# Kernel tuning notes

Hardware: AMD Instinct MI355X
Metric: run time of the kernel (lower is better)

Reference implementation:

```python
import jax, jax.numpy as jnp
import numpy as np

IM_SIZE = (384, 384)
GRID_OVERSAMP = 1.25
GRID_SIZE = tuple(round(s * GRID_OVERSAMP) for s in IM_SIZE)  # (480, 480)
N, C, K = 1, 16, 500000


def setup_inputs() -> dict:
    key = jax.random.key(0)
    k1, k2, k3 = jax.random.split(key, 3)
    img_real = jax.random.normal(k1, (N, C) + IM_SIZE, dtype=jnp.float32)
    img_imag = jax.random.normal(k2, (N, C) + IM_SIZE, dtype=jnp.float32)
    # continuous k-space trajectory coords in [-s/2, s/2) per dim
    u = jax.random.uniform(k3, (N, K, 2), dtype=jnp.float32)
    trj = (u - 0.5) * jnp.asarray(IM_SIZE, dtype=jnp.float32)
    return {"img_real": img_real, "img_imag": img_imag, "trj": trj}


def _rescale_trajectory(trj):
    # trj * oversamp, shift to [0, gs-1], round -> int32 grid indices
    gs = jnp.asarray(GRID_SIZE, dtype=jnp.float32)
    trj_rs = trj * GRID_OVERSAMP
    trj_rs = jnp.clip(trj_rs + gs / 2, 0.0, gs - 1)
    return jnp.round(trj_rs).astype(jnp.int32)


def _forward_complex(img, idx):
    # PadLast: center-pad last d dims from im_size to grid size
    pads = [((g - s) // 2, g - s - (g - s) // 2) for g, s in zip(GRID_SIZE, IM_SIZE)]
    img_os = jnp.pad(img, ((0, 0), (0, 0), pads[0], pads[1]))
    # sp_fft: centered orthonormal FFT over spatial dims
    axes = (-2, -1)
    ksp_os = jnp.fft.fftshift(
        jnp.fft.fftn(jnp.fft.ifftshift(img_os, axes=axes), axes=axes, norm="ortho"),
        axes=axes,
    )  # (N, C, Gx, Gy) complex64
    # per-batch irregular gather at rounded grid indices (multi_index)
    gather = jax.vmap(lambda k, t: k[:, t[:, 0], t[:, 1]])(ksp_os, idx)  # (N, C, K)
    return gather


def reference(img_real, img_imag, trj):
    img = (img_real + 1j * img_imag).astype(jnp.complex64)
    idx = _rescale_trajectory(trj)
    ksp = _forward_complex(img, idx)
    # return real/imag stacked so output is a float tensor: (2, N, C, K)
    return jnp.stack([ksp.real, ksp.imag]).astype(jnp.float32)
```

## Files before the change

### kernel.cpp

```cpp
#include <hip/hip_runtime.h>
#include <math.h>

#define PI_F 3.14159265358979323846f
#define LROW 489

__device__ __forceinline__ void wave_sync() {
  __builtin_amdgcn_wave_barrier();
  asm volatile("" ::: "memory");
}

__device__ __forceinline__ void dft2(float* vr, float* vi) {
  float ar = vr[0], ai = vi[0];
  vr[0] = ar + vr[1]; vi[0] = ai + vi[1];
  vr[1] = ar - vr[1]; vi[1] = ai - vi[1];
}

__device__ __forceinline__ void dft3(float* vr, float* vi) {
  const float s3 = 0.86602540378443864676f;
  float t1r = vr[1] + vr[2], t1i = vi[1] + vi[2];
  float t2r = vr[1] - vr[2], t2i = vi[1] - vi[2];
  float ar = vr[0] - 0.5f * t1r, ai = vi[0] - 0.5f * t1i;
  float br = s3 * t2r, bi = s3 * t2i;
  vr[0] = vr[0] + t1r; vi[0] = vi[0] + t1i;
  vr[1] = ar + bi; vi[1] = ai - br;
  vr[2] = ar - bi; vi[2] = ai + br;
}

__device__ __forceinline__ void dft4(float* vr, float* vi) {
  float t0r = vr[0] + vr[2], t0i = vi[0] + vi[2];
  float t1r = vr[0] - vr[2], t1i = vi[0] - vi[2];
  float t2r = vr[1] + vr[3], t2i = vi[1] + vi[3];
  float t3r = vr[1] - vr[3], t3i = vi[1] - vi[3];
  vr[0] = t0r + t2r; vi[0] = t0i + t2i;
  vr[2] = t0r - t2r; vi[2] = t0i - t2i;
  vr[1] = t1r + t3i; vi[1] = t1i - t3r;
  vr[3] = t1r - t3i; vi[3] = t1i + t3r;
}

__device__ __forceinline__ void dft5(float* vr, float* vi) {
  const float c1 = 0.30901699437494742410f, s1 = 0.95105651629515357212f;
  const float c2 = -0.80901699437494742410f, s2 = 0.58778525229247312917f;
  float t1r = vr[1] + vr[4], t1i = vi[1] + vi[4];
  float t2r = vr[2] + vr[3], t2i = vi[2] + vi[3];
  float t3r = vr[1] - vr[4], t3i = vi[1] - vi[4];
  float t4r = vr[2] - vr[3], t4i = vi[2] - vi[3];
  float a1r = vr[0] + c1 * t1r + c2 * t2r, a1i = vi[0] + c1 * t1i + c2 * t2i;
  float a2r = vr[0] + c2 * t1r + c1 * t2r, a2i = vi[0] + c2 * t1i + c1 * t2i;
  float b1r = s1 * t3r + s2 * t4r, b1i = s1 * t3i + s2 * t4i;
  float b2r = s2 * t3r - s1 * t4r, b2i = s2 * t3i - s1 * t4i;
  vr[0] = vr[0] + t1r + t2r; vi[0] = vi[0] + t1i + t2i;
  vr[1] = a1r + b1i; vi[1] = a1i - b1r;
  vr[4] = a1r - b1i; vi[4] = a1i + b1r;
  vr[2] = a2r + b2i; vi[2] = a2i - b2r;
  vr[3] = a2r - b2i; vi[3] = a2i + b2r;
}

__device__ __forceinline__ void dft8(float* vr, float* vi) {
  float er[4]  = {vr[0], vr[2], vr[4], vr[6]};
  float ei[4]  = {vi[0], vi[2], vi[4], vi[6]};
  float or_[4] = {vr[1], vr[3], vr[5], vr[7]};
  float oi[4]  = {vi[1], vi[3], vi[5], vi[7]};
  dft4(er, ei); dft4(or_, oi);
  const float h = 0.70710678118654752440f;
  float t1r = h * (or_[1] + oi[1]), t1i = h * (oi[1] - or_[1]);
  float t2r = oi[2],                t2i = -or_[2];
  float t3r = h * (oi[3] - or_[3]), t3i = -h * (or_[3] + oi[3]);
  vr[0] = er[0] + or_[0]; vi[0] = ei[0] + oi[0];
  vr[4] = er[0] - or_[0]; vi[4] = ei[0] - oi[0];
  vr[1] = er[1] + t1r;    vi[1] = ei[1] + t1i;
  vr[5] = er[1] - t1r;    vi[5] = ei[1] - t1i;
  vr[2] = er[2] + t2r;    vi[2] = ei[2] + t2i;
  vr[6] = er[2] - t2r;    vi[6] = ei[2] - t2i;
  vr[3] = er[3] + t3r;    vi[3] = ei[3] + t3i;
  vr[7] = er[3] - t3r;    vi[7] = ei[3] - t3i;
}

template <int R, int Ls>
__device__ __forceinline__ void fft_stage_ip(float2* s, int lane) {
  constexpr int M = 480 / R;
  constexpr int NI = (M + 63) / 64;
  const float w = -2.0f * PI_F / (float)(Ls * R);
  float vr[NI][R], vi[NI][R];
#pragma unroll
  for (int t = 0; t < NI; ++t) {
    const int i = lane + t * 64;
    if (i < M) {
#pragma unroll
      for (int r = 0; r < R; ++r) {
        float2 x = s[i + r * M];
        vr[t][r] = x.x; vi[t][r] = x.y;
      }
    }
  }
  asm volatile("" ::: "memory");
#pragma unroll
  for (int t = 0; t < NI; ++t) {
    const int i = lane + t * 64;
    if (i < M) {
      const int j = i % Ls, k = i / Ls;
      if constexpr (Ls > 1) {
#pragma unroll
        for (int r = 1; r < R; ++r) {
          float sn, cs;
          __sincosf(w * (float)(j * r), &sn, &cs);
          float tr = vr[t][r] * cs - vi[t][r] * sn;
          vi[t][r] = vr[t][r] * sn + vi[t][r] * cs;
          vr[t][r] = tr;
        }
      }
      if constexpr (R == 2) dft2(vr[t], vi[t]);
      else if constexpr (R == 3) dft3(vr[t], vi[t]);
      else if constexpr (R == 4) dft4(vr[t], vi[t]);
      else if constexpr (R == 5) dft5(vr[t], vi[t]);
      else dft8(vr[t], vi[t]);
      const int base = k * (Ls * R) + j;
#pragma unroll
      for (int r = 0; r < R; ++r)
        s[base + r * Ls] = make_float2(vr[t][r], vi[t][r]);
    }
  }
}

__device__ __forceinline__ void fft480_ip(float2* s, int lane) {
  fft_stage_ip<5, 1>(s, lane);    wave_sync();
  fft_stage_ip<8, 5>(s, lane);    wave_sync();
  fft_stage_ip<4, 40>(s, lane);   wave_sync();
  fft_stage_ip<3, 160>(s, lane);
}

__global__ __launch_bounds__(512) void pass1_kernel(const float* __restrict__ imgr,
                                                    const float* __restrict__ imgi,
                                                    float2* __restrict__ A) {
  __shared__ float2 s[8][LROW];
  const int lb = threadIdx.x >> 6, lane = threadIdx.x & 63;
  const int g0 = blockIdx.x * 8;
  const int c = g0 / 384, x0 = g0 % 384;
  const int xp = x0 + lb;
  const float* rowr = imgr + (size_t)(c * 384 + xp) * 384;
  const float* rowi = imgi + (size_t)(c * 384 + xp) * 384;
  float2* srow = &s[lb][0];

  for (int y = lane; y < 480; y += 64) {
    float r = 0.f, im = 0.f;
    if (y >= 48 && y < 432) {
      const int yp = y - 48;
      const float sgn = ((xp + yp) & 1) ? -1.f : 1.f;
      r = rowr[yp] * sgn; im = rowi[yp] * sgn;
    }
    srow[y] = make_float2(r, im);
  }
  wave_sync();
  fft480_ip(srow, lane);
  __syncthreads();
  for (int e = threadIdx.x; e < 480 * 8; e += 512) {
    const int v = e >> 3, xb = e & 7;
    A[((size_t)(c * 480 + v)) * 384 + (x0 + xb)] = s[xb][v];
  }
}

__global__ __launch_bounds__(512) void pass2_kernel(const float2* __restrict__ A,
                                                    float2* __restrict__ B) {
  __shared__ float2 s[8][LROW];
  const int lb = threadIdx.x >> 6, lane = threadIdx.x & 63;
  const int v = blockIdx.x >> 1, half = blockIdx.x & 1;
  const int c = half * 8 + lb;
  const float2* Arow = A + ((size_t)(c * 480 + v)) * 384;
  float2* srow = &s[lb][0];

  for (int x = lane; x < 480; x += 64) {
    float r = 0.f, im = 0.f;
    if (x >= 48 && x < 432) { float2 t = Arow[x - 48]; r = t.x; im = t.y; }
    srow[x] = make_float2(r, im);
  }
  wave_sync();
  fft480_ip(srow, lane);
  __syncthreads();
  const float inv = 1.0f / 480.0f;
  for (int e = threadIdx.x; e < 480 * 8; e += 512) {
    const int u = e >> 3, w2 = e & 7;
    float2 t = s[w2][u];
    B[((size_t)v * 480 + u) * 16 + half * 8 + w2] = make_float2(t.x * inv, t.y * inv);
  }
}

__global__ __launch_bounds__(256) void gather_kernel(const float2* __restrict__ B,
                                                     const float* __restrict__ trj,
                                                     float* __restrict__ out) {
  const int k = blockIdx.x * 256 + threadIdx.x;
  if (k >= 500000) return;
  const float2 t = ((const float2*)trj)[k];
  float p0 = t.x * 1.25f;
  float p1 = t.y * 1.25f;
  asm volatile("" : "+v"(p0), "+v"(p1));
  float v0 = p0 + 240.0f;
  float v1 = p1 + 240.0f;
  v0 = fminf(fmaxf(v0, 0.0f), 479.0f);
  v1 = fminf(fmaxf(v1, 0.0f), 479.0f);
  const int i0 = (int)rintf(v0);
  const int i1 = (int)rintf(v1);
  const float scale = ((i0 + i1) & 1) ? -1.0f : 1.0f;
  const float4* cell = (const float4*)(B + ((size_t)i1 * 480 + i0) * 16);
#pragma unroll
  for (int cc = 0; cc < 8; ++cc) {
    float4 q = cell[cc];
    const int c = 2 * cc;
    __builtin_nontemporal_store(q.x * scale, &out[(size_t)c * 500000 + k]);
    __builtin_nontemporal_store(q.y * scale, &out[8000000 + (size_t)c * 500000 + k]);
    __builtin_nontemporal_store(q.z * scale, &out[(size_t)(c + 1) * 500000 + k]);
    __builtin_nontemporal_store(q.w * scale, &out[8000000 + (size_t)(c + 1) * 500000 + k]);
  }
}

extern "C" void kernel_launch(void* const* d_in, const int* in_sizes, int n_in,
                              void* d_out, int out_size, void* d_ws, size_t ws_size,
                              hipStream_t stream) {
  const float* imgr = (const float*)d_in[0];
  const float* imgi = (const float*)d_in[1];
  const float* trj  = (const float*)d_in[2];
  float* out = (float*)d_out;

  const size_t A_floats = (size_t)16 * 384 * 480 * 2;
  float2* A = (float2*)(out + (16000000 - A_floats));
  float2* B = (float2*)d_ws;

  hipLaunchKernelGGL(pass1_kernel, dim3(16 * 384 / 8), dim3(512), 0, stream, imgr, imgi, A);
  hipLaunchKernelGGL(pass2_kernel, dim3(480 * 2), dim3(512), 0, stream, A, B);
  hipLaunchKernelGGL(gather_kernel, dim3((500000 + 255) / 256), dim3(256), 0, stream,
                     B, trj, out);
}
```

Measured before the change: 123.0 us.

## Stage spectrum in output buffer and gate gather stores with grid barrier

The intermediate spectrum B now lives in the tail of the output buffer rather than the workspace, and A sits at its start. The gather kernel first loads every sample into registers, then waits on a global atomic counter until all blocks have loaded before writing output, so no store can overwrite B while it is still being read. The goal is to keep the intermediates in one buffer that stays in cache and to drop the separate workspace. This relies on all 977 blocks of 512 threads being resident at the same time, otherwise the spin barrier deadlocks. It also adds an extra memset launch and a grid-wide sync.

```diff
diff --git a/kernel.cpp b/kernel.cpp
--- a/kernel.cpp
+++ b/kernel.cpp
@@ -183,31 +183,48 @@
   }
 }
 
-__global__ __launch_bounds__(256) void gather_kernel(const float2* __restrict__ B,
-                                                     const float* __restrict__ trj,
-                                                     float* __restrict__ out) {
-  const int k = blockIdx.x * 256 + threadIdx.x;
-  if (k >= 500000) return;
-  const float2 t = ((const float2*)trj)[k];
-  float p0 = t.x * 1.25f;
-  float p1 = t.y * 1.25f;
-  asm volatile("" : "+v"(p0), "+v"(p1));
-  float v0 = p0 + 240.0f;
-  float v1 = p1 + 240.0f;
-  v0 = fminf(fmaxf(v0, 0.0f), 479.0f);
-  v1 = fminf(fmaxf(v1, 0.0f), 479.0f);
-  const int i0 = (int)rintf(v0);
-  const int i1 = (int)rintf(v1);
-  const float scale = ((i0 + i1) & 1) ? -1.0f : 1.0f;
-  const float4* cell = (const float4*)(B + ((size_t)i1 * 480 + i0) * 16);
-#pragma unroll
-  for (int cc = 0; cc < 8; ++cc) {
-    float4 q = cell[cc];
-    const int c = 2 * cc;
-    __builtin_nontemporal_store(q.x * scale, &out[(size_t)c * 500000 + k]);
-    __builtin_nontemporal_store(q.y * scale, &out[8000000 + (size_t)c * 500000 + k]);
-    __builtin_nontemporal_store(q.z * scale, &out[(size_t)(c + 1) * 500000 + k]);
-    __builtin_nontemporal_store(q.w * scale, &out[8000000 + (size_t)(c + 1) * 500000 + k]);
+#define GBLK 977
+__global__ __launch_bounds__(512, 8) void gather_kernel(const float2* __restrict__ B,
+                                                        const float* __restrict__ trj,
+                                                        float* __restrict__ out,
+                                                        unsigned* __restrict__ cnt) {
+  const int k = blockIdx.x * 512 + threadIdx.x;
+  const bool act = (k < 500000);
+  float4 q[8];
+  float scale = 1.0f;
+  if (act) {
+    const float2 t = ((const float2*)trj)[k];
+    float p0 = t.x * 1.25f;
+    float p1 = t.y * 1.25f;
+    asm volatile("" : "+v"(p0), "+v"(p1));
+    float v0 = p0 + 240.0f;
+    float v1 = p1 + 240.0f;
+    v0 = fminf(fmaxf(v0, 0.0f), 479.0f);
+    v1 = fminf(fmaxf(v1, 0.0f), 479.0f);
+    const int i0 = (int)rintf(v0);
+    const int i1 = (int)rintf(v1);
+    scale = ((i0 + i1) & 1) ? -1.0f : 1.0f;
+    const float4* cell = (const float4*)(B + ((size_t)i1 * 480 + i0) * 16);
+#pragma unroll
+    for (int cc = 0; cc < 8; ++cc) q[cc] = cell[cc];
+  }
+  __syncthreads();
+  if (threadIdx.x == 0) {
+    __hip_atomic_fetch_add(cnt, 1u, __ATOMIC_ACQ_REL, __HIP_MEMORY_SCOPE_AGENT);
+    while (__hip_atomic_load(cnt, __ATOMIC_ACQUIRE, __HIP_MEMORY_SCOPE_AGENT) <
+           (unsigned)GBLK)
+      __builtin_amdgcn_s_sleep(2);
+  }
+  __syncthreads();
+  if (act) {
+#pragma unroll
+    for (int cc = 0; cc < 8; ++cc) {
+      const int c = 2 * cc;
+      __builtin_nontemporal_store(q[cc].x * scale, &out[(size_t)c * 500000 + k]);
+      __builtin_nontemporal_store(q[cc].y * scale, &out[8000000 + (size_t)c * 500000 + k]);
+      __builtin_nontemporal_store(q[cc].z * scale, &out[(size_t)(c + 1) * 500000 + k]);
+      __builtin_nontemporal_store(q[cc].w * scale, &out[8000000 + (size_t)(c + 1) * 500000 + k]);
+    }
   }
 }
 
@@ -219,12 +236,14 @@
   const float* trj  = (const float*)d_in[2];
   float* out = (float*)d_out;
 
-  const size_t A_floats = (size_t)16 * 384 * 480 * 2;
-  float2* A = (float2*)(out + (16000000 - A_floats));
-  float2* B = (float2*)d_ws;
-
+  (void)d_ws; (void)ws_size;
+  const size_t B_floats = (size_t)480 * 480 * 16 * 2;
+  float2* A = (float2*)(out + 2);
+  float2* B = (float2*)(out + (16000000 - B_floats));
+  unsigned* cnt = (unsigned*)out;
+
+  hipMemsetAsync(out, 0, 4, stream);
   hipLaunchKernelGGL(pass1_kernel, dim3(16 * 384 / 8), dim3(512), 0, stream, imgr, imgi, A);
   hipLaunchKernelGGL(pass2_kernel, dim3(480 * 2), dim3(512), 0, stream, A, B);
-  hipLaunchKernelGGL(gather_kernel, dim3((500000 + 255) / 256), dim3(256), 0, stream,
-                     B, trj, out);
-}
+  hipLaunchKernelGGL(gather_kernel, dim3(GBLK), dim3(512), 0, stream, B, trj, out, cnt);
+}
```

Result: slower. 244.2 us (+98.6%).
